# Kernel optimization log

Hardware: AMD Instinct MI355X
Metric: run time of the kernel (lower is better)

The kernel has to match this reference:

```python
import jax, jax.numpy as jnp
import numpy as np


def _cdist(x, y):
    # x: (b, n, c), y: (b, m, c) -> (b, n, m) Euclidean distances
    x2 = jnp.sum(x * x, axis=-1, keepdims=True)          # (b, n, 1)
    y2 = jnp.sum(y * y, axis=-1)[:, None, :]             # (b, 1, m)
    xy = jnp.einsum('bnc,bmc->bnm', x, y)                # (b, n, m)
    d2 = jnp.maximum(x2 + y2 - 2.0 * xy, 0.0)
    return jnp.sqrt(d2)


def setup_inputs() -> dict:
    key = jax.random.key(0)
    k1, k2, k3, k4 = jax.random.split(key, 4)
    bs, N, M, C = 8, 4096, 4096, 128
    return {
        'set1': jax.random.normal(k1, (bs, N, C), dtype=jnp.float32),
        'set2': jax.random.normal(k2, (bs, M, C), dtype=jnp.float32),
        'w1': jax.random.uniform(k3, (bs, N), dtype=jnp.float32),
        'w2': jax.random.uniform(k4, (bs, M), dtype=jnp.float32),
    }


def reference(set1, set2, w1, w2):
    dist = _cdist(set1, set2)                 # (b, N, M)
    out_dist = jnp.min(dist, axis=2)          # (b, N)
    out_dist2 = jnp.min(dist, axis=1)         # (b, M)
    total = (jnp.sum(w1 * out_dist) + jnp.sum(w2 * out_dist2)) / 2.0
    return total
```

## Files before the change

### kernel.cpp

```cpp
#include <hip/hip_runtime.h>

#define BS 8
#define NN 4096
#define MM 4096
#define CC 128
#define XT 128
#define YT 128
#define MH 2048
#define NMT (MH / YT)
#define NPH (2 * NMT)
#define NXT (NN / XT)
#define SLICE (YT * 64)

#define FINF_BITS 0x7F800000u

typedef __attribute__((ext_vector_type(8))) short bf16x8;
typedef __attribute__((ext_vector_type(4))) float f32x4;

#define WAITVn(n) asm volatile("s_waitcnt vmcnt(" #n ")" ::: "memory")
#define SCHED_FENCE() __builtin_amdgcn_sched_barrier(0)

__device__ inline ushort f2bf(float f) {
    unsigned u = __float_as_uint(f);
    unsigned r = (u + 0x7FFFu + ((u >> 16) & 1u)) >> 16;
    return (ushort)r;
}

__global__ void ch_prep(const float* __restrict__ y,
                        ushort* __restrict__ y16, float* __restrict__ yn,
                        unsigned* __restrict__ rowmin, unsigned* __restrict__ colmin,
                        float* __restrict__ out) {
    int gid = blockIdx.x * blockDim.x + threadIdx.x;
    size_t i = (size_t)gid * 8;

    float4 w0 = *(const float4*)(y + i);
    float4 w1 = *(const float4*)(y + i + 4);
    ushort h[8] = {f2bf(w0.x), f2bf(w0.y), f2bf(w0.z), f2bf(w0.w),
                   f2bf(w1.x), f2bf(w1.y), f2bf(w1.z), f2bf(w1.w)};
    *(bf16x8*)(y16 + i) = *(bf16x8*)h;
    float sy = w0.x * w0.x + w0.y * w0.y + w0.z * w0.z + w0.w * w0.w +
               w1.x * w1.x + w1.y * w1.y + w1.z * w1.z + w1.w * w1.w;

#pragma unroll
    for (int mask = 1; mask <= 8; mask <<= 1)
        sy += __shfl_xor(sy, mask, 64);
    if ((threadIdx.x & 15) == 0)
        yn[gid >> 4] = sy;

    if (gid < BS * NN) rowmin[gid] = FINF_BITS;
    if (gid < BS * MM) colmin[gid] = FINF_BITS;
    if (gid == 0) out[0] = 0.0f;
}

__device__ __forceinline__ void stage_y(const ushort* __restrict__ Yb,
                                        ushort* __restrict__ buf,
                                        int tile, int half, int tid, int wave) {
#pragma unroll
    for (int s = 0; s < 4; ++s) {
        int f = s * 256 + tid;
        int r = f >> 3, cslot = f & 7;
        const ushort* g = Yb + (size_t)(tile * YT + r) * CC + half * 64 +
                          ((cslot ^ (r & 7)) * 8);
        ushort* l = buf + (size_t)(s * 256 + wave * 64) * 8;
        __builtin_amdgcn_global_load_lds(
            (const __attribute__((address_space(1))) void*)g,
            (__attribute__((address_space(3))) void*)l, 16, 0, 0);
    }
}

__global__ __launch_bounds__(256, 2) void ch_tile(
    const float* __restrict__ Xf, const ushort* __restrict__ Y,
    const float* __restrict__ yn,
    unsigned* __restrict__ rowmin, unsigned* __restrict__ colmin) {

    __shared__ ushort pool[3 * SLICE];
    __shared__ unsigned coltile[MH];
    __shared__ unsigned rowtile[XT];
    __shared__ float xnorm[XT];
    __shared__ float ynld[MH];

    const int b  = blockIdx.x;
    const int xt = blockIdx.y;
    const int mh = blockIdx.z;
    const int n0 = xt * XT;
    const int m0 = mh * MH;
    const int tid  = threadIdx.x;
    const int lane = tid & 63;
    const int wave = tid >> 6;
    const int lc   = lane & 15;
    const int quad = lane >> 4;
    const int wm = wave >> 1;
    const int wn = wave & 1;

    const ushort* Yb = Y + ((size_t)b * MM + m0) * CC;

    ushort* xs = pool;
    const float* Xb = Xf + ((size_t)b * NN + n0) * CC;
    {
        float psum[8];
#pragma unroll
        for (int s = 0; s < 8; ++s) {
            int flat = s * 256 + tid;
            int r = flat >> 4, c = flat & 15;
            float4 v0 = *(const float4*)(Xb + (size_t)r * CC + c * 8);
            float4 v1 = *(const float4*)(Xb + (size_t)r * CC + c * 8 + 4);
            ushort h[8] = {f2bf(v0.x), f2bf(v0.y), f2bf(v0.z), f2bf(v0.w),
                           f2bf(v1.x), f2bf(v1.y), f2bf(v1.z), f2bf(v1.w)};
            *(bf16x8*)(xs + r * CC + (c ^ (r & 7)) * 8) = *(bf16x8*)h;
            psum[s] = v0.x * v0.x + v0.y * v0.y + v0.z * v0.z + v0.w * v0.w +
                      v1.x * v1.x + v1.y * v1.y + v1.z * v1.z + v1.w * v1.w;
        }
#pragma unroll
        for (int mask = 1; mask <= 8; mask <<= 1)
#pragma unroll
            for (int s = 0; s < 8; ++s)
                psum[s] += __shfl_xor(psum[s], mask, 64);
        if ((tid & 15) == 0) {
#pragma unroll
            for (int s = 0; s < 8; ++s)
                xnorm[s * 16 + (tid >> 4)] = psum[s];
        }
    }
    {
        const float* ynb = yn + (size_t)b * MM + m0;
#pragma unroll
        for (int s = 0; s < MH / 256; ++s)
            ynld[s * 256 + tid] = ynb[s * 256 + tid];
    }
    for (int c2 = tid; c2 < MH; c2 += 256) coltile[c2] = FINF_BITS;
    if (tid < XT) rowtile[tid] = FINF_BITS;

    __syncthreads();

    bf16x8 af[4][4];
    const int xrow = (wm * 64 + lc) * CC;
    const int xsw  = lc & 7;
#pragma unroll
    for (int kt = 0; kt < 4; ++kt)
#pragma unroll
        for (int i = 0; i < 4; ++i)
            af[kt][i] = *(const bf16x8*)(xs + xrow + i * 16 * CC +
                                         ((kt * 4 + quad) ^ xsw) * 8);

    float xnp[4][4];
#pragma unroll
    for (int i = 0; i < 4; ++i) {
        float4 t = *(const float4*)(&xnorm[wm * 64 + i * 16 + quad * 4]);
        xnp[i][0] = t.x; xnp[i][1] = t.y; xnp[i][2] = t.z; xnp[i][3] = t.w;
    }
    float rm[4][4];
#pragma unroll
    for (int i = 0; i < 4; ++i)
#pragma unroll
        for (int r = 0; r < 4; ++r) rm[i][r] = __builtin_inff();

    __syncthreads();

    stage_y(Yb, pool + 0 * SLICE, 0, 0, tid, wave);
    stage_y(Yb, pool + 1 * SLICE, 0, 1, tid, wave);
    WAITVn(4);
    __builtin_amdgcn_s_barrier();
    SCHED_FENCE();

    int rd = 0;
#pragma unroll 1
    for (int t = 0; t < NMT; ++t) {
        f32x4 acc[4][4];
        const f32x4 z = {0.f, 0.f, 0.f, 0.f};
        float ynr[4];

        {
            const int ph = 2 * t;
            const ushort* ybuf = pool + rd * SLICE;
            if (ph + 2 < NPH) {
                int wr = rd + 2; if (wr >= 3) wr -= 3;
                stage_y(Yb, pool + wr * SLICE, (ph + 2) >> 1, (ph + 2) & 1,
                        tid, wave);
            }
#pragma unroll
            for (int j = 0; j < 4; ++j)
                ynr[j] = ynld[t * YT + wn * 64 + j * 16 + lc];
#pragma unroll
            for (int s2 = 0; s2 < 2; ++s2) {
                bf16x8 yf[4];
                const int cy = ((s2 * 4 + quad) ^ xsw) * 8;
#pragma unroll
                for (int j = 0; j < 4; ++j)
                    yf[j] = *(const bf16x8*)(ybuf + (wn * 64 + j * 16 + lc) * 64 + cy);
                __builtin_amdgcn_s_setprio(1);
#pragma unroll
                for (int j = 0; j < 4; ++j)
#pragma unroll
                    for (int i = 0; i < 4; ++i)
                        acc[i][j] = __builtin_amdgcn_mfma_f32_16x16x32_bf16(
                            af[s2][i], yf[j], (s2 == 0) ? z : acc[i][j], 0, 0, 0);
                __builtin_amdgcn_s_setprio(0);
            }
            SCHED_FENCE();
            if (ph + 2 < NPH) { WAITVn(4); } else { WAITVn(0); }
            __builtin_amdgcn_s_barrier();
            SCHED_FENCE();
            rd = (rd == 2) ? 0 : rd + 1;
        }

        {
            const int ph = 2 * t + 1;
            const ushort* ybuf = pool + rd * SLICE;
            if (ph + 2 < NPH) {
                int wr = rd + 2; if (wr >= 3) wr -= 3;
                stage_y(Yb, pool + wr * SLICE, (ph + 2) >> 1, (ph + 2) & 1,
                        tid, wave);
            }
#pragma unroll
            for (int s2 = 0; s2 < 2; ++s2) {
                bf16x8 yf[4];
                const int cy = ((s2 * 4 + quad) ^ xsw) * 8;
#pragma unroll
                for (int j = 0; j < 4; ++j)
                    yf[j] = *(const bf16x8*)(ybuf + (wn * 64 + j * 16 + lc) * 64 + cy);
                __builtin_amdgcn_s_setprio(1);
#pragma unroll
                for (int j = 0; j < 4; ++j)
#pragma unroll
                    for (int i = 0; i < 4; ++i)
                        acc[i][j] = __builtin_amdgcn_mfma_f32_16x16x32_bf16(
                            af[2 + s2][i], yf[j], acc[i][j], 0, 0, 0);
                __builtin_amdgcn_s_setprio(0);
            }

            float cmv[4];
#pragma unroll
            for (int j = 0; j < 4; ++j) cmv[j] = __builtin_inff();
#pragma unroll
            for (int i = 0; i < 4; ++i) {
#pragma unroll
                for (int j = 0; j < 4; ++j) {
                    f32x4 a = acc[i][j];
                    float e[4];
#pragma unroll
                    for (int r = 0; r < 4; ++r)
                        e[r] = xnp[i][r] + fmaf(-2.0f, a[r], ynr[j]);
#pragma unroll
                    for (int r = 0; r < 4; ++r)
                        rm[i][r] = fminf(rm[i][r], e[r]);
                    cmv[j] = fminf(cmv[j],
                                   fminf(fminf(e[0], e[1]), fminf(e[2], e[3])));
                }
            }
#pragma unroll
            for (int mask = 16; mask <= 32; mask <<= 1)
#pragma unroll
                for (int j = 0; j < 4; ++j)
                    cmv[j] = fminf(cmv[j], __shfl_xor(cmv[j], mask, 64));
            if (quad == 0) {
#pragma unroll
                for (int j = 0; j < 4; ++j)
                    atomicMin(&coltile[t * YT + wn * 64 + j * 16 + lc],
                              __float_as_uint(fmaxf(cmv[j], 0.0f)));
            }

            SCHED_FENCE();
            if (ph + 2 < NPH) { WAITVn(4); } else { WAITVn(0); }
            __builtin_amdgcn_s_barrier();
            SCHED_FENCE();
            rd = (rd == 2) ? 0 : rd + 1;
        }
    }

#pragma unroll
    for (int mask = 1; mask <= 8; mask <<= 1)
#pragma unroll
        for (int i = 0; i < 4; ++i)
#pragma unroll
            for (int r = 0; r < 4; ++r)
                rm[i][r] = fminf(rm[i][r], __shfl_xor(rm[i][r], mask, 64));
    if (lc == 0) {
#pragma unroll
        for (int i = 0; i < 4; ++i)
#pragma unroll
            for (int r = 0; r < 4; ++r)
                atomicMin(&rowtile[wm * 64 + i * 16 + quad * 4 + r],
                          __float_as_uint(fmaxf(rm[i][r], 0.0f)));
    }

    __syncthreads();
    if (tid < XT)
        atomicMin(&rowmin[(size_t)b * NN + n0 + tid], rowtile[tid]);
    for (int c2 = tid; c2 < MH; c2 += 256)
        atomicMin(&colmin[(size_t)b * MM + m0 + c2], coltile[c2]);
}

__global__ void ch_finalize(const unsigned* __restrict__ rowmin,
                            const unsigned* __restrict__ colmin,
                            const float* __restrict__ w1,
                            const float* __restrict__ w2,
                            float* __restrict__ out) {
    int i = blockIdx.x * blockDim.x + threadIdx.x;
    int stride = gridDim.x * blockDim.x;
    float s = 0.f;
    for (int idx = i; idx < BS * NN; idx += stride)
        s += w1[idx] * sqrtf(__uint_as_float(rowmin[idx])) +
             w2[idx] * sqrtf(__uint_as_float(colmin[idx]));
#pragma unroll
    for (int off = 32; off > 0; off >>= 1) s += __shfl_down(s, off, 64);
    __shared__ float ls[4];
    int lane = threadIdx.x & 63, wv = threadIdx.x >> 6;
    if (lane == 0) ls[wv] = s;
    __syncthreads();
    if (threadIdx.x == 0) {
        float t = ls[0] + ls[1] + ls[2] + ls[3];
        atomicAdd(out, 0.5f * t);
    }
}

extern "C" void kernel_launch(void* const* d_in, const int* in_sizes, int n_in,
                              void* d_out, int out_size, void* d_ws, size_t ws_size,
                              hipStream_t stream) {
    const float* set1 = (const float*)d_in[0];
    const float* set2 = (const float*)d_in[1];
    const float* w1   = (const float*)d_in[2];
    const float* w2   = (const float*)d_in[3];
    float* out = (float*)d_out;

    ushort*   y16    = (ushort*)d_ws;
    float*    yn     = (float*)(y16 + (size_t)BS * MM * CC);
    unsigned* rowmin = (unsigned*)(yn + BS * MM);
    unsigned* colmin = rowmin + BS * NN;

    ch_prep<<<BS * MM * CC / 8 / 256, 256, 0, stream>>>(
        set2, y16, yn, rowmin, colmin, out);

    dim3 grid(BS, NXT, MM / MH);
    ch_tile<<<grid, 256, 0, stream>>>(set1, y16, yn, rowmin, colmin);

    ch_finalize<<<64, 256, 0, stream>>>(rowmin, colmin, w1, w2, out);
}
```

Measured before the change: 125.4 us.

## Software-pipeline epilogue of previous tile under MFMAs of the next tile

Double-buffers the MFMA accumulators (accA/accB) so the distance/min epilogue and column atomicMin flush for tile t-1 are interleaved with the MFMA chain of tile t, rather than run serially after it. The loop is unrolled by two with ping-pong register sets plus a prologue and a drained epilogue. The aim is to hide VALU epilogue latency behind matrix-core work. The cost is doubled accumulator registers (64 extra VGPR/AGPR), which risks lower occupancy or spills.

```diff
diff --git a/kernel.cpp b/kernel.cpp
--- a/kernel.cpp
+++ b/kernel.cpp
@@ -163,27 +163,74 @@
     SCHED_FENCE();
 
     int rd = 0;
-#pragma unroll 1
-    for (int t = 0; t < NMT; ++t) {
-        f32x4 acc[4][4];
-        const f32x4 z = {0.f, 0.f, 0.f, 0.f};
-        float ynr[4];
-
+    const f32x4 z = {0.f, 0.f, 0.f, 0.f};
+    f32x4 accA[4][4], accB[4][4];
+    float ynrA[4], ynrB[4];
+
+    auto stage_q = [&](int ph) {
+        if (ph + 2 < NPH) {
+            int wr = rd + 2; if (wr >= 3) wr -= 3;
+            stage_y(Yb, pool + wr * SLICE, (ph + 2) >> 1, (ph + 2) & 1,
+                    tid, wave);
+        }
+    };
+    auto end_ph = [&](int ph) {
+        SCHED_FENCE();
+        if (ph + 2 < NPH) { WAITVn(4); } else { WAITVn(0); }
+        __builtin_amdgcn_s_barrier();
+        SCHED_FENCE();
+        rd = (rd == 2) ? 0 : rd + 1;
+    };
+
+    auto epi_arith = [&](f32x4 (&pa)[4][4], float (&pyn)[4], float (&cmv)[4]) {
+#pragma unroll
+        for (int j = 0; j < 4; ++j) cmv[j] = __builtin_inff();
+#pragma unroll
+        for (int i = 0; i < 4; ++i) {
+#pragma unroll
+            for (int j = 0; j < 4; ++j) {
+                f32x4 a = pa[i][j];
+                float e0 = xnp[i][0] + fmaf(-2.0f, a[0], pyn[j]);
+                float e1 = xnp[i][1] + fmaf(-2.0f, a[1], pyn[j]);
+                float e2 = xnp[i][2] + fmaf(-2.0f, a[2], pyn[j]);
+                float e3 = xnp[i][3] + fmaf(-2.0f, a[3], pyn[j]);
+                rm[i][0] = fminf(rm[i][0], e0);
+                rm[i][1] = fminf(rm[i][1], e1);
+                rm[i][2] = fminf(rm[i][2], e2);
+                rm[i][3] = fminf(rm[i][3], e3);
+                cmv[j] = fminf(cmv[j],
+                               fminf(fminf(e0, e1), fminf(e2, e3)));
+            }
+        }
+    };
+    auto epi_flush = [&](float (&cmv)[4], int tprev) {
+#pragma unroll
+        for (int mask = 16; mask <= 32; mask <<= 1)
+#pragma unroll
+            for (int j = 0; j < 4; ++j)
+                cmv[j] = fminf(cmv[j], __shfl_xor(cmv[j], mask, 64));
+        if (quad == 0) {
+#pragma unroll
+            for (int j = 0; j < 4; ++j)
+                atomicMin(&coltile[tprev * YT + wn * 64 + j * 16 + lc],
+                          __float_as_uint(fmaxf(cmv[j], 0.0f)));
+        }
+    };
+
+    auto do_tile = [&](int t, f32x4 (&cacc)[4][4], float (&cyn)[4],
+                       f32x4 (&pacc)[4][4], float (&pyn)[4],
+                       bool do_epi, int tprev) {
+        float cmv[4];
         {
             const int ph = 2 * t;
             const ushort* ybuf = pool + rd * SLICE;
-            if (ph + 2 < NPH) {
-                int wr = rd + 2; if (wr >= 3) wr -= 3;
-                stage_y(Yb, pool + wr * SLICE, (ph + 2) >> 1, (ph + 2) & 1,
-                        tid, wave);
-            }
+            stage_q(ph);
 #pragma unroll
             for (int j = 0; j < 4; ++j)
-                ynr[j] = ynld[t * YT + wn * 64 + j * 16 + lc];
-#pragma unroll
-            for (int s2 = 0; s2 < 2; ++s2) {
+                cyn[j] = ynld[t * YT + wn * 64 + j * 16 + lc];
+            {
                 bf16x8 yf[4];
-                const int cy = ((s2 * 4 + quad) ^ xsw) * 8;
+                const int cy = ((0 + quad) ^ xsw) * 8;
 #pragma unroll
                 for (int j = 0; j < 4; ++j)
                     yf[j] = *(const bf16x8*)(ybuf + (wn * 64 + j * 16 + lc) * 64 + cy);
@@ -192,29 +239,35 @@
                 for (int j = 0; j < 4; ++j)
 #pragma unroll
                     for (int i = 0; i < 4; ++i)
-                        acc[i][j] = __builtin_amdgcn_mfma_f32_16x16x32_bf16(
-                            af[s2][i], yf[j], (s2 == 0) ? z : acc[i][j], 0, 0, 0);
+                        cacc[i][j] = __builtin_amdgcn_mfma_f32_16x16x32_bf16(
+                            af[0][i], yf[j], z, 0, 0, 0);
                 __builtin_amdgcn_s_setprio(0);
             }
-            SCHED_FENCE();
-            if (ph + 2 < NPH) { WAITVn(4); } else { WAITVn(0); }
-            __builtin_amdgcn_s_barrier();
-            SCHED_FENCE();
-            rd = (rd == 2) ? 0 : rd + 1;
-        }
-
+            {
+                bf16x8 yf[4];
+                const int cy = ((4 + quad) ^ xsw) * 8;
+#pragma unroll
+                for (int j = 0; j < 4; ++j)
+                    yf[j] = *(const bf16x8*)(ybuf + (wn * 64 + j * 16 + lc) * 64 + cy);
+                if (do_epi) epi_arith(pacc, pyn, cmv);
+                __builtin_amdgcn_s_setprio(1);
+#pragma unroll
+                for (int j = 0; j < 4; ++j)
+#pragma unroll
+                    for (int i = 0; i < 4; ++i)
+                        cacc[i][j] = __builtin_amdgcn_mfma_f32_16x16x32_bf16(
+                            af[1][i], yf[j], cacc[i][j], 0, 0, 0);
+                __builtin_amdgcn_s_setprio(0);
+            }
+            end_ph(ph);
+        }
         {
             const int ph = 2 * t + 1;
             const ushort* ybuf = pool + rd * SLICE;
-            if (ph + 2 < NPH) {
-                int wr = rd + 2; if (wr >= 3) wr -= 3;
-                stage_y(Yb, pool + wr * SLICE, (ph + 2) >> 1, (ph + 2) & 1,
-                        tid, wave);
-            }
-#pragma unroll
-            for (int s2 = 0; s2 < 2; ++s2) {
+            stage_q(ph);
+            {
                 bf16x8 yf[4];
-                const int cy = ((s2 * 4 + quad) ^ xsw) * 8;
+                const int cy = ((0 + quad) ^ xsw) * 8;
 #pragma unroll
                 for (int j = 0; j < 4; ++j)
                     yf[j] = *(const bf16x8*)(ybuf + (wn * 64 + j * 16 + lc) * 64 + cy);
@@ -223,48 +276,42 @@
                 for (int j = 0; j < 4; ++j)
 #pragma unroll
                     for (int i = 0; i < 4; ++i)
-                        acc[i][j] = __builtin_amdgcn_mfma_f32_16x16x32_bf16(
-                            af[2 + s2][i], yf[j], acc[i][j], 0, 0, 0);
+                        cacc[i][j] = __builtin_amdgcn_mfma_f32_16x16x32_bf16(
+                            af[2][i], yf[j], cacc[i][j], 0, 0, 0);
                 __builtin_amdgcn_s_setprio(0);
             }
-
-            float cmv[4];
-#pragma unroll
-            for (int j = 0; j < 4; ++j) cmv[j] = __builtin_inff();
-#pragma unroll
-            for (int i = 0; i < 4; ++i) {
-#pragma unroll
-                for (int j = 0; j < 4; ++j) {
-                    f32x4 a = acc[i][j];
-                    float e[4];
-#pragma unroll
-                    for (int r = 0; r < 4; ++r)
-                        e[r] = xnp[i][r] + fmaf(-2.0f, a[r], ynr[j]);
-#pragma unroll
-                    for (int r = 0; r < 4; ++r)
-                        rm[i][r] = fminf(rm[i][r], e[r]);
-                    cmv[j] = fminf(cmv[j],
-                                   fminf(fminf(e[0], e[1]), fminf(e[2], e[3])));
-                }
-            }
-#pragma unroll
-            for (int mask = 16; mask <= 32; mask <<= 1)
-#pragma unroll
-                for (int j = 0; j < 4; ++j)
-                    cmv[j] = fminf(cmv[j], __shfl_xor(cmv[j], mask, 64));
-            if (quad == 0) {
-#pragma unroll
-                for (int j = 0; j < 4; ++j)
-                    atomicMin(&coltile[t * YT + wn * 64 + j * 16 + lc],
-                              __float_as_uint(fmaxf(cmv[j], 0.0f)));
-            }
-
-            SCHED_FENCE();
-            if (ph + 2 < NPH) { WAITVn(4); } else { WAITVn(0); }
-            __builtin_amdgcn_s_barrier();
-            SCHED_FENCE();
-            rd = (rd == 2) ? 0 : rd + 1;
-        }
+            {
+                bf16x8 yf[4];
+                const int cy = ((4 + quad) ^ xsw) * 8;
+#pragma unroll
+                for (int j = 0; j < 4; ++j)
+                    yf[j] = *(const bf16x8*)(ybuf + (wn * 64 + j * 16 + lc) * 64 + cy);
+                if (do_epi) epi_flush(cmv, tprev);
+                __builtin_amdgcn_s_setprio(1);
+#pragma unroll
+                for (int j = 0; j < 4; ++j)
+#pragma unroll
+                    for (int i = 0; i < 4; ++i)
+                        cacc[i][j] = __builtin_amdgcn_mfma_f32_16x16x32_bf16(
+                            af[3][i], yf[j], cacc[i][j], 0, 0, 0);
+                __builtin_amdgcn_s_setprio(0);
+            }
+            end_ph(ph);
+        }
+    };
+
+    do_tile(0, accA, ynrA, accB, ynrB, false, 0);
+#pragma unroll 1
+    for (int t = 1; t + 2 < NMT; t += 2) {
+        do_tile(t,     accB, ynrB, accA, ynrA, true, t - 1);
+        do_tile(t + 1, accA, ynrA, accB, ynrB, true, t);
+    }
+    do_tile(NMT - 1, accB, ynrB, accA, ynrA, true, NMT - 2);
+
+    {
+        float cmv[4];
+        epi_arith(accB, ynrB, cmv);
+        epi_flush(cmv, NMT - 1);
     }
 
 #pragma unroll
```

Result: slower. 274.9 us (+119.2%).

## Overlap min-reduction epilogue of previous tile with MFMA clusters of next tile

Applied to the files above, without the earlier changes.

Double-buffers the MFMA accumulators (accA/accB) so the distance epilogue for tile t-1 (row/column minimum updates) is interleaved between the MFMA clusters of tile t. The idea is to hide VALU epilogue work behind matrix-core execution instead of running it serially after each tile. It also drops the per-element x-norm add from the row-min path and applies it once at the end, and reads x-norms from LDS on demand rather than keeping them in registers. Holding two accumulator sets doubles accumulator register use, which at launch bounds (256,2) risks spills or lower occupancy.

```diff
diff --git a/kernel.cpp b/kernel.cpp
--- a/kernel.cpp
+++ b/kernel.cpp
@@ -67,6 +67,117 @@
             (__attribute__((address_space(3))) void*)l, 16, 0, 0);
     }
 }
+
+
+#define CLUSTER(CACC, KT, S2, FIRST)                                          \
+    {                                                                         \
+        const int cy_ = (((S2) * 4 + quad) ^ xsw) * 8;                        \
+        bf16x8 yf0_ = *(const bf16x8*)(ybuf_ + (wn * 64 +  0 + lc) * 64 + cy_);\
+        bf16x8 yf1_ = *(const bf16x8*)(ybuf_ + (wn * 64 + 16 + lc) * 64 + cy_);\
+        bf16x8 yf2_ = *(const bf16x8*)(ybuf_ + (wn * 64 + 32 + lc) * 64 + cy_);\
+        bf16x8 yf3_ = *(const bf16x8*)(ybuf_ + (wn * 64 + 48 + lc) * 64 + cy_);\
+        __builtin_amdgcn_s_setprio(1);                                        \
+        _Pragma("unroll")                                                     \
+        for (int i_ = 0; i_ < 4; ++i_) {                                      \
+            CACC[i_][0] = __builtin_amdgcn_mfma_f32_16x16x32_bf16(            \
+                af[KT][i_], yf0_, (FIRST) ? z : CACC[i_][0], 0, 0, 0);        \
+            CACC[i_][1] = __builtin_amdgcn_mfma_f32_16x16x32_bf16(            \
+                af[KT][i_], yf1_, (FIRST) ? z : CACC[i_][1], 0, 0, 0);        \
+            CACC[i_][2] = __builtin_amdgcn_mfma_f32_16x16x32_bf16(            \
+                af[KT][i_], yf2_, (FIRST) ? z : CACC[i_][2], 0, 0, 0);        \
+            CACC[i_][3] = __builtin_amdgcn_mfma_f32_16x16x32_bf16(            \
+                af[KT][i_], yf3_, (FIRST) ? z : CACC[i_][3], 0, 0, 0);        \
+        }                                                                     \
+        __builtin_amdgcn_s_setprio(0);                                        \
+        SCHED_FENCE();                                                        \
+    }
+
+#define EPI_LOAD(TPREV)                                                       \
+    {                                                                         \
+        _Pragma("unroll")                                                     \
+        for (int j_ = 0; j_ < 4; ++j_) {                                      \
+            pyn[j_] = ynld[(TPREV) * YT + wn * 64 + j_ * 16 + lc];            \
+            cmv[j_] = __builtin_inff();                                       \
+        }                                                                     \
+    }
+
+#define EPI_PART(PACC, I)                                                     \
+    {                                                                         \
+        float4 xq_ = *(const float4*)(&xnorm[wm * 64 + (I) * 16 + quad * 4]); \
+        _Pragma("unroll")                                                     \
+        for (int j_ = 0; j_ < 4; ++j_) {                                      \
+            f32x4 a_ = PACC[I][j_];                                           \
+            float g0_ = fmaf(-2.0f, a_[0], pyn[j_]);                          \
+            float g1_ = fmaf(-2.0f, a_[1], pyn[j_]);                          \
+            float g2_ = fmaf(-2.0f, a_[2], pyn[j_]);                          \
+            float g3_ = fmaf(-2.0f, a_[3], pyn[j_]);                          \
+            rm[I][0] = fminf(rm[I][0], g0_);                                  \
+            rm[I][1] = fminf(rm[I][1], g1_);                                  \
+            rm[I][2] = fminf(rm[I][2], g2_);                                  \
+            rm[I][3] = fminf(rm[I][3], g3_);                                  \
+            float m01_ = fminf(xq_.x + g0_, xq_.y + g1_);                     \
+            float m23_ = fminf(xq_.z + g2_, xq_.w + g3_);                     \
+            cmv[j_] = fminf(cmv[j_], fminf(m01_, m23_));                      \
+        }                                                                     \
+    }
+
+#define EPI_FLUSH(TPREV)                                                      \
+    {                                                                         \
+        _Pragma("unroll")                                                     \
+        for (int mask_ = 16; mask_ <= 32; mask_ <<= 1)                        \
+            _Pragma("unroll")                                                 \
+            for (int j_ = 0; j_ < 4; ++j_)                                    \
+                cmv[j_] = fminf(cmv[j_], __shfl_xor(cmv[j_], mask_, 64));     \
+        if (quad == 0) {                                                      \
+            _Pragma("unroll")                                                 \
+            for (int j_ = 0; j_ < 4; ++j_)                                    \
+                atomicMin(&coltile[(TPREV) * YT + wn * 64 + j_ * 16 + lc],    \
+                          __float_as_uint(fmaxf(cmv[j_], 0.0f)));             \
+        }                                                                     \
+    }
+
+#define END_PH(PH)                                                            \
+    {                                                                         \
+        SCHED_FENCE();                                                        \
+        if ((PH) + 2 < NPH) { WAITVn(4); } else { WAITVn(0); }                \
+        __builtin_amdgcn_s_barrier();                                         \
+        SCHED_FENCE();                                                        \
+        rd = (rd == 2) ? 0 : rd + 1;                                          \
+    }
+
+#define STAGE_Q(PH)                                                           \
+    if ((PH) + 2 < NPH) {                                                     \
+        int wr_ = rd + 2; if (wr_ >= 3) wr_ -= 3;                             \
+        stage_y(Yb, pool + wr_ * SLICE, ((PH) + 2) >> 1, ((PH) + 2) & 1,      \
+                tid, wave);                                                   \
+    }
+
+#define DO_TILE(T, CACC, PACC, DOEPI, TPREV)                                  \
+    {                                                                         \
+        float pyn[4], cmv[4];                                                 \
+        {                                        \
+            const int ph_ = 2 * (T);                                          \
+            const ushort* ybuf_ = pool + rd * SLICE;                          \
+            STAGE_Q(ph_);                                                     \
+            if (DOEPI) EPI_LOAD(TPREV);                                       \
+            CLUSTER(CACC, 0, 0, true);                                        \
+            if (DOEPI) EPI_PART(PACC, 0);                                     \
+            CLUSTER(CACC, 1, 1, false);                                       \
+            if (DOEPI) EPI_PART(PACC, 1);                                     \
+            END_PH(ph_);                                                      \
+        }                                                                     \
+        {                                        \
+            const int ph_ = 2 * (T) + 1;                                      \
+            const ushort* ybuf_ = pool + rd * SLICE;                          \
+            STAGE_Q(ph_);                                                     \
+            CLUSTER(CACC, 2, 0, false);                                       \
+            if (DOEPI) EPI_PART(PACC, 2);                                     \
+            CLUSTER(CACC, 3, 1, false);                                       \
+            if (DOEPI) EPI_PART(PACC, 3);                                     \
+            if (DOEPI) EPI_FLUSH(TPREV);                                      \
+            END_PH(ph_);                                                      \
+        }                                                                     \
+    }
 
 __global__ __launch_bounds__(256, 2) void ch_tile(
     const float* __restrict__ Xf, const ushort* __restrict__ Y,
@@ -142,12 +253,6 @@
             af[kt][i] = *(const bf16x8*)(xs + xrow + i * 16 * CC +
                                          ((kt * 4 + quad) ^ xsw) * 8);
 
-    float xnp[4][4];
-#pragma unroll
-    for (int i = 0; i < 4; ++i) {
-        float4 t = *(const float4*)(&xnorm[wm * 64 + i * 16 + quad * 4]);
-        xnp[i][0] = t.x; xnp[i][1] = t.y; xnp[i][2] = t.z; xnp[i][3] = t.w;
-    }
     float rm[4][4];
 #pragma unroll
     for (int i = 0; i < 4; ++i)
@@ -163,108 +268,25 @@
     SCHED_FENCE();
 
     int rd = 0;
+    const f32x4 z = {0.f, 0.f, 0.f, 0.f};
+    f32x4 accA[4][4], accB[4][4];
+
+    DO_TILE(0, accA, accB, 0, 0);
 #pragma unroll 1
-    for (int t = 0; t < NMT; ++t) {
-        f32x4 acc[4][4];
-        const f32x4 z = {0.f, 0.f, 0.f, 0.f};
-        float ynr[4];
-
-        {
-            const int ph = 2 * t;
-            const ushort* ybuf = pool + rd * SLICE;
-            if (ph + 2 < NPH) {
-                int wr = rd + 2; if (wr >= 3) wr -= 3;
-                stage_y(Yb, pool + wr * SLICE, (ph + 2) >> 1, (ph + 2) & 1,
-                        tid, wave);
-            }
-#pragma unroll
-            for (int j = 0; j < 4; ++j)
-                ynr[j] = ynld[t * YT + wn * 64 + j * 16 + lc];
-#pragma unroll
-            for (int s2 = 0; s2 < 2; ++s2) {
-                bf16x8 yf[4];
-                const int cy = ((s2 * 4 + quad) ^ xsw) * 8;
-#pragma unroll
-                for (int j = 0; j < 4; ++j)
-                    yf[j] = *(const bf16x8*)(ybuf + (wn * 64 + j * 16 + lc) * 64 + cy);
-                __builtin_amdgcn_s_setprio(1);
-#pragma unroll
-                for (int j = 0; j < 4; ++j)
-#pragma unroll
-                    for (int i = 0; i < 4; ++i)
-                        acc[i][j] = __builtin_amdgcn_mfma_f32_16x16x32_bf16(
-                            af[s2][i], yf[j], (s2 == 0) ? z : acc[i][j], 0, 0, 0);
-                __builtin_amdgcn_s_setprio(0);
-            }
-            SCHED_FENCE();
-            if (ph + 2 < NPH) { WAITVn(4); } else { WAITVn(0); }
-            __builtin_amdgcn_s_barrier();
-            SCHED_FENCE();
-            rd = (rd == 2) ? 0 : rd + 1;
-        }
-
-        {
-            const int ph = 2 * t + 1;
-            const ushort* ybuf = pool + rd * SLICE;
-            if (ph + 2 < NPH) {
-                int wr = rd + 2; if (wr >= 3) wr -= 3;
-                stage_y(Yb, pool + wr * SLICE, (ph + 2) >> 1, (ph + 2) & 1,
-                        tid, wave);
-            }
-#pragma unroll
-            for (int s2 = 0; s2 < 2; ++s2) {
-                bf16x8 yf[4];
-                const int cy = ((s2 * 4 + quad) ^ xsw) * 8;
-#pragma unroll
-                for (int j = 0; j < 4; ++j)
-                    yf[j] = *(const bf16x8*)(ybuf + (wn * 64 + j * 16 + lc) * 64 + cy);
-                __builtin_amdgcn_s_setprio(1);
-#pragma unroll
-                for (int j = 0; j < 4; ++j)
-#pragma unroll
-                    for (int i = 0; i < 4; ++i)
-                        acc[i][j] = __builtin_amdgcn_mfma_f32_16x16x32_bf16(
-                            af[2 + s2][i], yf[j], acc[i][j], 0, 0, 0);
-                __builtin_amdgcn_s_setprio(0);
-            }
-
-            float cmv[4];
-#pragma unroll
-            for (int j = 0; j < 4; ++j) cmv[j] = __builtin_inff();
-#pragma unroll
-            for (int i = 0; i < 4; ++i) {
-#pragma unroll
-                for (int j = 0; j < 4; ++j) {
-                    f32x4 a = acc[i][j];
-                    float e[4];
-#pragma unroll
-                    for (int r = 0; r < 4; ++r)
-                        e[r] = xnp[i][r] + fmaf(-2.0f, a[r], ynr[j]);
-#pragma unroll
-                    for (int r = 0; r < 4; ++r)
-                        rm[i][r] = fminf(rm[i][r], e[r]);
-                    cmv[j] = fminf(cmv[j],
-                                   fminf(fminf(e[0], e[1]), fminf(e[2], e[3])));
-                }
-            }
-#pragma unroll
-            for (int mask = 16; mask <= 32; mask <<= 1)
-#pragma unroll
-                for (int j = 0; j < 4; ++j)
-                    cmv[j] = fminf(cmv[j], __shfl_xor(cmv[j], mask, 64));
-            if (quad == 0) {
-#pragma unroll
-                for (int j = 0; j < 4; ++j)
-                    atomicMin(&coltile[t * YT + wn * 64 + j * 16 + lc],
-                              __float_as_uint(fmaxf(cmv[j], 0.0f)));
-            }
-
-            SCHED_FENCE();
-            if (ph + 2 < NPH) { WAITVn(4); } else { WAITVn(0); }
-            __builtin_amdgcn_s_barrier();
-            SCHED_FENCE();
-            rd = (rd == 2) ? 0 : rd + 1;
-        }
+    for (int t = 1; t + 1 < NMT; t += 2) {
+        DO_TILE(t,     accB, accA, 1, t - 1);
+        DO_TILE(t + 1, accA, accB, 1, t);
+    }
+    DO_TILE(NMT - 1, accB, accA, 1, NMT - 2);
+
+    {
+        float pyn[4], cmv[4];
+        EPI_LOAD(NMT - 1);
+        EPI_PART(accB, 0);
+        EPI_PART(accB, 1);
+        EPI_PART(accB, 2);
+        EPI_PART(accB, 3);
+        EPI_FLUSH(NMT - 1);
     }
 
 #pragma unroll
@@ -276,11 +298,14 @@
                 rm[i][r] = fminf(rm[i][r], __shfl_xor(rm[i][r], mask, 64));
     if (lc == 0) {
 #pragma unroll
-        for (int i = 0; i < 4; ++i)
+        for (int i = 0; i < 4; ++i) {
+            float4 xq = *(const float4*)(&xnorm[wm * 64 + i * 16 + quad * 4]);
+            float xr[4] = {xq.x, xq.y, xq.z, xq.w};
 #pragma unroll
             for (int r = 0; r < 4; ++r)
                 atomicMin(&rowtile[wm * 64 + i * 16 + quad * 4 + r],
-                          __float_as_uint(fmaxf(rm[i][r], 0.0f)));
+                          __float_as_uint(fmaxf(rm[i][r] + xr[r], 0.0f)));
+        }
     }
 
     __syncthreads();
```

Result: slower. 244.9 us (+95.3%).

## Switch Y staging to full-tile double buffering with one barrier per tile and halve MH

Applied to the files above, without the earlier changes.

Replaces the three-slot, half-tile ring buffer, which had a barrier after each half-K phase, with two full-tile buffers. The next tile is prefetched during compute, and each tile needs one wait and one barrier. MH is halved, which doubles the grid along the M split and shortens each block's loop. The aim is fewer barriers and more blocks for better occupancy and load balance. The costs are more LDS per block, which may limit blocks per CU, more global atomic merges of the partial column and row minima, and a coarser prefetch that waits on all loads every iteration.

```diff
diff --git a/kernel.cpp b/kernel.cpp
--- a/kernel.cpp
+++ b/kernel.cpp
@@ -6,9 +6,8 @@
 #define CC 128
 #define XT 128
 #define YT 128
-#define MH 2048
+#define MH 1024
 #define NMT (MH / YT)
-#define NPH (2 * NMT)
 #define NXT (NN / XT)
 #define SLICE (YT * 64)
 
@@ -73,7 +72,7 @@
     const float* __restrict__ yn,
     unsigned* __restrict__ rowmin, unsigned* __restrict__ colmin) {
 
-    __shared__ ushort pool[3 * SLICE];
+    __shared__ ushort pool[4 * SLICE];
     __shared__ unsigned coltile[MH];
     __shared__ unsigned rowtile[XT];
     __shared__ float xnorm[XT];
@@ -158,30 +157,34 @@
 
     stage_y(Yb, pool + 0 * SLICE, 0, 0, tid, wave);
     stage_y(Yb, pool + 1 * SLICE, 0, 1, tid, wave);
-    WAITVn(4);
+    WAITVn(0);
     __builtin_amdgcn_s_barrier();
     SCHED_FENCE();
 
-    int rd = 0;
+    const f32x4 z = {0.f, 0.f, 0.f, 0.f};
+
 #pragma unroll 1
     for (int t = 0; t < NMT; ++t) {
+        const ushort* ybase = pool + (t & 1) * (2 * SLICE);
+
+        if (t + 1 < NMT) {
+            ushort* wbase = pool + ((t + 1) & 1) * (2 * SLICE);
+            stage_y(Yb, wbase, t + 1, 0, tid, wave);
+            stage_y(Yb, wbase + SLICE, t + 1, 1, tid, wave);
+        }
+
+        float ynr[4];
+#pragma unroll
+        for (int j = 0; j < 4; ++j)
+            ynr[j] = ynld[t * YT + wn * 64 + j * 16 + lc];
+
         f32x4 acc[4][4];
-        const f32x4 z = {0.f, 0.f, 0.f, 0.f};
-        float ynr[4];
-
-        {
-            const int ph = 2 * t;
-            const ushort* ybuf = pool + rd * SLICE;
-            if (ph + 2 < NPH) {
-                int wr = rd + 2; if (wr >= 3) wr -= 3;
-                stage_y(Yb, pool + wr * SLICE, (ph + 2) >> 1, (ph + 2) & 1,
-                        tid, wave);
-            }
-#pragma unroll
-            for (int j = 0; j < 4; ++j)
-                ynr[j] = ynld[t * YT + wn * 64 + j * 16 + lc];
+#pragma unroll
+        for (int h = 0; h < 2; ++h) {
+            const ushort* ybuf = ybase + h * SLICE;
 #pragma unroll
             for (int s2 = 0; s2 < 2; ++s2) {
+                const int ktg = h * 2 + s2;
                 bf16x8 yf[4];
                 const int cy = ((s2 * 4 + quad) ^ xsw) * 8;
 #pragma unroll
@@ -193,78 +196,46 @@
 #pragma unroll
                     for (int i = 0; i < 4; ++i)
                         acc[i][j] = __builtin_amdgcn_mfma_f32_16x16x32_bf16(
-                            af[s2][i], yf[j], (s2 == 0) ? z : acc[i][j], 0, 0, 0);
+                            af[ktg][i], yf[j], (ktg == 0) ? z : acc[i][j], 0, 0, 0);
                 __builtin_amdgcn_s_setprio(0);
             }
-            SCHED_FENCE();
-            if (ph + 2 < NPH) { WAITVn(4); } else { WAITVn(0); }
-            __builtin_amdgcn_s_barrier();
-            SCHED_FENCE();
-            rd = (rd == 2) ? 0 : rd + 1;
-        }
-
-        {
-            const int ph = 2 * t + 1;
-            const ushort* ybuf = pool + rd * SLICE;
-            if (ph + 2 < NPH) {
-                int wr = rd + 2; if (wr >= 3) wr -= 3;
-                stage_y(Yb, pool + wr * SLICE, (ph + 2) >> 1, (ph + 2) & 1,
-                        tid, wave);
+        }
+
+        float cmv[4];
+#pragma unroll
+        for (int j = 0; j < 4; ++j) cmv[j] = __builtin_inff();
+#pragma unroll
+        for (int i = 0; i < 4; ++i) {
+#pragma unroll
+            for (int j = 0; j < 4; ++j) {
+                f32x4 a = acc[i][j];
+                float e[4];
+#pragma unroll
+                for (int r = 0; r < 4; ++r)
+                    e[r] = xnp[i][r] + fmaf(-2.0f, a[r], ynr[j]);
+#pragma unroll
+                for (int r = 0; r < 4; ++r)
+                    rm[i][r] = fminf(rm[i][r], e[r]);
+                cmv[j] = fminf(cmv[j],
+                               fminf(fminf(e[0], e[1]), fminf(e[2], e[3])));
             }
-#pragma unroll
-            for (int s2 = 0; s2 < 2; ++s2) {
-                bf16x8 yf[4];
-                const int cy = ((s2 * 4 + quad) ^ xsw) * 8;
-#pragma unroll
-                for (int j = 0; j < 4; ++j)
-                    yf[j] = *(const bf16x8*)(ybuf + (wn * 64 + j * 16 + lc) * 64 + cy);
-                __builtin_amdgcn_s_setprio(1);
-#pragma unroll
-                for (int j = 0; j < 4; ++j)
-#pragma unroll
-                    for (int i = 0; i < 4; ++i)
-                        acc[i][j] = __builtin_amdgcn_mfma_f32_16x16x32_bf16(
-                            af[2 + s2][i], yf[j], acc[i][j], 0, 0, 0);
-                __builtin_amdgcn_s_setprio(0);
-            }
-
-            float cmv[4];
-#pragma unroll
-            for (int j = 0; j < 4; ++j) cmv[j] = __builtin_inff();
-#pragma unroll
-            for (int i = 0; i < 4; ++i) {
-#pragma unroll
-                for (int j = 0; j < 4; ++j) {
-                    f32x4 a = acc[i][j];
-                    float e[4];
-#pragma unroll
-                    for (int r = 0; r < 4; ++r)
-                        e[r] = xnp[i][r] + fmaf(-2.0f, a[r], ynr[j]);
-#pragma unroll
-                    for (int r = 0; r < 4; ++r)
-                        rm[i][r] = fminf(rm[i][r], e[r]);
-                    cmv[j] = fminf(cmv[j],
-                                   fminf(fminf(e[0], e[1]), fminf(e[2], e[3])));
-                }
-            }
-#pragma unroll
-            for (int mask = 16; mask <= 32; mask <<= 1)
-#pragma unroll
-                for (int j = 0; j < 4; ++j)
-                    cmv[j] = fminf(cmv[j], __shfl_xor(cmv[j], mask, 64));
-            if (quad == 0) {
-#pragma unroll
-                for (int j = 0; j < 4; ++j)
-                    atomicMin(&coltile[t * YT + wn * 64 + j * 16 + lc],
-                              __float_as_uint(fmaxf(cmv[j], 0.0f)));
-            }
-
-            SCHED_FENCE();
-            if (ph + 2 < NPH) { WAITVn(4); } else { WAITVn(0); }
-            __builtin_amdgcn_s_barrier();
-            SCHED_FENCE();
-            rd = (rd == 2) ? 0 : rd + 1;
-        }
+        }
+#pragma unroll
+        for (int mask = 16; mask <= 32; mask <<= 1)
+#pragma unroll
+            for (int j = 0; j < 4; ++j)
+                cmv[j] = fminf(cmv[j], __shfl_xor(cmv[j], mask, 64));
+        if (quad == 0) {
+#pragma unroll
+            for (int j = 0; j < 4; ++j)
+                atomicMin(&coltile[t * YT + wn * 64 + j * 16 + lc],
+                          __float_as_uint(fmaxf(cmv[j], 0.0f)));
+        }
+
+        SCHED_FENCE();
+        WAITVn(0);
+        __builtin_amdgcn_s_barrier();
+        SCHED_FENCE();
     }
 
 #pragma unroll
```

After: 127.3 us. About the same (+1.5%).
